# Kernel optimization log

Hardware: AMD Instinct MI355X
Metric: run time of the kernel (lower is better)

## Reference

```python
import jax, jax.numpy as jnp
import numpy as np

N_NODES = 100000


def _gcn_layer(h, W, b, src, dst, norm, n):
    # h: [N, Fin] -> transform then normalized scatter-add aggregation
    h = h @ W                                   # [N, Fout]
    msg = h[src] * norm[:, None]                # [E', Fout] gather + scale
    out = jax.ops.segment_sum(msg, dst, num_segments=n)  # scatter-add
    return out + b


def setup_inputs() -> dict:
    key = jax.random.key(0)
    k1, k2, k3, k4 = jax.random.split(key, 4)
    N, F_IN, HID, C, E = N_NODES, 512, 128, 40, 1600000
    x = jax.random.normal(k1, (N, F_IN), dtype=jnp.float32)
    edge_index = jax.random.randint(k2, (2, E), 0, N, dtype=jnp.int64)
    W1 = jax.random.normal(k3, (F_IN, HID), dtype=jnp.float32) * (1.0 / np.sqrt(F_IN))
    b1 = jnp.zeros((HID,), dtype=jnp.float32)
    W2 = jax.random.normal(k4, (HID, C), dtype=jnp.float32) * (1.0 / np.sqrt(HID))
    b2 = jnp.zeros((C,), dtype=jnp.float32)
    return {"x": x, "edge_index": edge_index, "W1": W1, "b1": b1, "W2": W2, "b2": b2}


def reference(x, edge_index, W1, b1, W2, b2):
    n = x.shape[0]
    # add self-loops (GCNConv default)
    loop = jnp.arange(n, dtype=edge_index.dtype)
    src = jnp.concatenate([edge_index[0], loop])
    dst = jnp.concatenate([edge_index[1], loop])
    # symmetric normalization: deg counted on destination (in-degree, incl. self-loop)
    deg = jax.ops.segment_sum(jnp.ones_like(dst, dtype=x.dtype), dst, num_segments=n)
    dis = jnp.where(deg > 0, jax.lax.rsqrt(deg), 0.0)  # deg^{-1/2}
    norm = dis[src] * dis[dst]                          # per-edge weight

    h = jax.nn.relu(_gcn_layer(x, W1, b1, src, dst, norm, n))
    # dropout: identity in eval mode (training=False)
    h = _gcn_layer(h, W2, b2, src, dst, norm, n)
    return jax.nn.log_softmax(h, axis=1)
```

## Files before the change

### kernel.cpp

```cpp
#include <hip/hip_runtime.h>
#include <hip/hip_bf16.h>


#define F_IN 512
#define HID  128
#define NC   40
#define NCP  48

typedef __attribute__((ext_vector_type(8))) short bf16x8;
typedef __attribute__((ext_vector_type(4))) float f32x4v;

__device__ __forceinline__ ushort f2bf(float f) {
    unsigned r;
    asm("v_cvt_pk_bf16_f32 %0, %1, %1" : "=v"(r) : "v"(f));
    return (ushort)r;
}
__device__ __forceinline__ unsigned cvtpk(float a, float b) {
    unsigned r;
    asm("v_cvt_pk_bf16_f32 %0, %1, %2" : "=v"(r) : "v"(a), "v"(b));
    return r;
}
__device__ __forceinline__ float bf2f(ushort u) {
    return __uint_as_float((unsigned)u << 16);
}
__device__ __forceinline__ bf16x8 cvt8(float4 lo, float4 hi) {
    union { unsigned u[4]; bf16x8 v; } t;
    t.u[0] = cvtpk(lo.x, lo.y); t.u[1] = cvtpk(lo.z, lo.w);
    t.u[2] = cvtpk(hi.x, hi.y); t.u[3] = cvtpk(hi.z, hi.w);
    return t.v;
}

__global__ void prep_k(const int* __restrict__ dst, int E, int EB,
                       unsigned* __restrict__ cnt, int* __restrict__ rank,
                       const float* __restrict__ W1, const float* __restrict__ W2,
                       ushort* __restrict__ W1p, ushort* __restrict__ W2p) {
    int b = blockIdx.x;
    if (b < EB) {
        int t = b * 256 + threadIdx.x;
        if (t < E) rank[t] = (int)atomicAdd(&cnt[dst[t]], 1u);
        return;
    }
    int t = (b - EB) * 256 + threadIdx.x;
    if (t < 65536) {
        int j = t & 7, n = (t >> 3) & 127, kb = (t >> 10) & 3, s = t >> 12;
        int k = s * 32 + kb * 8 + j;
        W1p[t] = f2bf(W1[(size_t)k * HID + n]);
    } else {
        int q = t - 65536;
        if (q < 6144) {
            int j = q & 7;
            int i2 = q >> 3;
            int n = i2 % 48;
            int i3 = i2 / 48;
            int kb = i3 & 3, ks = i3 >> 2;
            int k = ks * 32 + kb * 8 + j;
            float v = (n < NC) ? W2[(size_t)k * NC + n] : 0.f;
            W2p[q] = f2bf(v);
        }
    }
}

__global__ __launch_bounds__(1024) void scan_block(const unsigned* __restrict__ cnt,
                                                   unsigned* __restrict__ offs,
                                                   unsigned* __restrict__ bsums,
                                                   float* __restrict__ dis, int N) {
    int tid = threadIdx.x;
    int i = blockIdx.x * 1024 + tid;
    unsigned v = (i < N) ? cnt[i] : 0u;
    if (i < N) dis[i] = rsqrtf((float)v + 1.0f);
    int lane = tid & 63, w = tid >> 6;
    unsigned s = v;
    #pragma unroll
    for (int d = 1; d < 64; d <<= 1) {
        unsigned t = __shfl_up(s, d, 64);
        if (lane >= d) s += t;
    }
    __shared__ unsigned wt[16];
    if (lane == 63) wt[w] = s;
    __syncthreads();
    unsigned add = 0;
    #pragma unroll
    for (int j = 0; j < 16; j++) add += (j < w) ? wt[j] : 0u;
    unsigned incl = s + add;
    if (i < N) offs[i] = incl - v;
    if (tid == 1023) bsums[blockIdx.x] = incl;
}

__global__ __launch_bounds__(1024) void scan_add2(unsigned* __restrict__ offs,
                                                  const unsigned* __restrict__ bsums,
                                                  int N, unsigned total) {
    int i = blockIdx.x * 1024 + threadIdx.x;
    int lane = threadIdx.x & 63;
    unsigned s = 0;
    for (int j = lane; j < (int)blockIdx.x; j += 64) s += bsums[j];
    #pragma unroll
    for (int d = 1; d < 64; d <<= 1) s += __shfl_xor(s, d, 64);
    if (i < N) offs[i] += s;
    if (i == 0) offs[N] = total;
}

__global__ __launch_bounds__(256) void fill_gemm1(
        const int* __restrict__ src, const int* __restrict__ dst,
        const unsigned* __restrict__ offs, const int* __restrict__ rank,
        int* __restrict__ col, int E, int GB,
        const float* __restrict__ A, const ushort* __restrict__ Bp,
        const float* __restrict__ dis, ushort* __restrict__ C, int N) {
    if (blockIdx.x >= GB) {
        int t = (blockIdx.x - GB) * 256 + threadIdx.x;
        if (t < E) {
            int d = dst[t];
            col[offs[d] + (unsigned)rank[t]] = src[t];
        }
        return;
    }
    const int tid  = threadIdx.x;
    const int wave = tid >> 6;
    const int lane = tid & 63;
    const int quad = lane >> 4;
    const int mr   = lane & 15;
    const int base = (blockIdx.x * 4 + wave) * 16;
    if (base >= N) return;
    const int r0 = base + mr;
    const bool ok0 = r0 < N;
    const float* ap0 = A + (size_t)(ok0 ? r0 : 0) * F_IN + quad * 8;
    const ushort* bp = Bp + quad * 1024 + mr * 8;

    f32x4v acc0[8];
    #pragma unroll
    for (int t = 0; t < 8; t++) acc0[t] = (f32x4v){0.f, 0.f, 0.f, 0.f};

    float4 av[4][2];
    #pragma unroll
    for (int b = 0; b < 4; b++) {
        av[b][0] = *(const float4*)(ap0 + b * 32);
        av[b][1] = *(const float4*)(ap0 + b * 32 + 4);
    }

    #pragma unroll
    for (int s = 0; s < 16; s++) {
        bf16x8 fa0 = cvt8(av[s & 3][0], av[s & 3][1]);
        if (s < 12) {
            av[s & 3][0] = *(const float4*)(ap0 + (s + 4) * 32);
            av[s & 3][1] = *(const float4*)(ap0 + (s + 4) * 32 + 4);
        }
        const ushort* bs = bp + s * 4096;
        #pragma unroll
        for (int t = 0; t < 8; t++) {
            bf16x8 b = *(const bf16x8*)(bs + t * 128);
            acc0[t] = __builtin_amdgcn_mfma_f32_16x16x32_bf16(fa0, b, acc0[t], 0, 0, 0);
        }
    }

    #pragma unroll
    for (int rr = 0; rr < 4; rr++) {
        int ra = base + quad * 4 + rr;
        if (ra < N) {
            float ds = dis[ra];
            #pragma unroll
            for (int t = 0; t < 8; t++)
                C[(size_t)ra * HID + t * 16 + mr] = f2bf(acc0[t][rr] * ds);
        }
    }
}

__global__ __launch_bounds__(256) void agg1_k(const ushort* __restrict__ h,
                                              const int* __restrict__ col,
                                              const unsigned* __restrict__ offs,
                                              const float* __restrict__ dis,
                                              const float* __restrict__ b1,
                                              ushort* __restrict__ out, int N) {
    int node = blockIdx.x * 4 + (threadIdx.x >> 6);
    if (node >= N) return;
    int lane = threadIdx.x & 63;
    int ni = lane >> 4;
    int fl = lane & 15;
    const ushort* hb = h + (size_t)fl * 8;
    float a[8] = {0.f, 0.f, 0.f, 0.f, 0.f, 0.f, 0.f, 0.f};
    if (ni == 0) {
        uint4 v = *(const uint4*)(hb + (size_t)node * HID);
        const ushort* u = (const ushort*)&v;
        #pragma unroll
        for (int j = 0; j < 8; j++) a[j] = bf2f(u[j]);
    }
    unsigned p0 = offs[node], p1 = offs[node + 1];
    int sA = (p0 + ni     < p1) ? col[p0 + ni]     : -1;
    int sB = (p0 + ni + 4 < p1) ? col[p0 + ni + 4] : -1;
    for (unsigned p = p0; p < p1; p += 8) {
        int sC = (p + 8 + ni  < p1) ? col[p + 8 + ni]  : -1;
        int sD = (p + 12 + ni < p1) ? col[p + 12 + ni] : -1;
        if (sA >= 0) {
            uint4 v = *(const uint4*)(hb + (size_t)sA * HID);
            const ushort* u = (const ushort*)&v;
            #pragma unroll
            for (int j = 0; j < 8; j++) a[j] += bf2f(u[j]);
        }
        if (sB >= 0) {
            uint4 v = *(const uint4*)(hb + (size_t)sB * HID);
            const ushort* u = (const ushort*)&v;
            #pragma unroll
            for (int j = 0; j < 8; j++) a[j] += bf2f(u[j]);
        }
        sA = sC; sB = sD;
    }
    #pragma unroll
    for (int j = 0; j < 8; j++) {
        a[j] += __shfl_xor(a[j], 16);
        a[j] += __shfl_xor(a[j], 32);
    }
    if (ni == 0) {
        float dd = dis[node];
        float4 bb0 = *(const float4*)(b1 + fl * 8);
        float4 bb1 = *(const float4*)(b1 + fl * 8 + 4);
        const float bb[8] = {bb0.x, bb0.y, bb0.z, bb0.w, bb1.x, bb1.y, bb1.z, bb1.w};
        __align__(16) ushort o[8];
        #pragma unroll
        for (int j = 0; j < 8; j++) o[j] = f2bf(fmaxf(a[j] * dd + bb[j], 0.f));
        *(uint4*)(out + (size_t)node * HID + (size_t)fl * 8) = *(const uint4*)o;
    }
}

__global__ __launch_bounds__(256) void gemm2_mfma(const ushort* __restrict__ A,
                                                  const ushort* __restrict__ W2p,
                                                  const float* __restrict__ dis,
                                                  ushort* __restrict__ h2, int N) {
    const int tid  = threadIdx.x;
    const int wave = tid >> 6;
    const int lane = tid & 63;
    const int quad = lane >> 4;
    const int mr   = lane & 15;
    const int base = (blockIdx.x * 4 + wave) * 32;
    if (base >= N) return;
    const int r0 = base + mr;
    const int r1 = base + 16 + mr;
    const bool ok0 = r0 < N, ok1 = r1 < N;
    const ushort* ap0 = A + (size_t)(ok0 ? r0 : 0) * HID + quad * 8;
    const ushort* ap1 = A + (size_t)(ok1 ? r1 : 0) * HID + quad * 8;
    const ushort* bp = W2p + quad * 384 + mr * 8;

    f32x4v acc0[3], acc1[3];
    #pragma unroll
    for (int t = 0; t < 3; t++) {
        acc0[t] = (f32x4v){0.f, 0.f, 0.f, 0.f};
        acc1[t] = (f32x4v){0.f, 0.f, 0.f, 0.f};
    }
    #pragma unroll
    for (int ks = 0; ks < 4; ks++) {
        bf16x8 a0 = *(const bf16x8*)(ap0 + ks * 32);
        bf16x8 a1 = *(const bf16x8*)(ap1 + ks * 32);
        #pragma unroll
        for (int t = 0; t < 3; t++) {
            bf16x8 b = *(const bf16x8*)(bp + ks * 1536 + t * 128);
            acc0[t] = __builtin_amdgcn_mfma_f32_16x16x32_bf16(a0, b, acc0[t], 0, 0, 0);
            acc1[t] = __builtin_amdgcn_mfma_f32_16x16x32_bf16(a1, b, acc1[t], 0, 0, 0);
        }
    }
    #pragma unroll
    for (int rr = 0; rr < 4; rr++) {
        int ra = base + quad * 4 + rr;
        if (ra < N) {
            float ds = dis[ra];
            #pragma unroll
            for (int t = 0; t < 3; t++) {
                int c = t * 16 + mr;
                if (c < NC) h2[(size_t)ra * NCP + c] = f2bf(acc0[t][rr] * ds);
            }
        }
        int rb = base + 16 + quad * 4 + rr;
        if (rb < N) {
            float ds = dis[rb];
            #pragma unroll
            for (int t = 0; t < 3; t++) {
                int c = t * 16 + mr;
                if (c < NC) h2[(size_t)rb * NCP + c] = f2bf(acc1[t][rr] * ds);
            }
        }
    }
}

__global__ __launch_bounds__(256) void agg2_ls(const ushort* __restrict__ h2,
                                               const int* __restrict__ col,
                                               const unsigned* __restrict__ offs,
                                               const float* __restrict__ dis,
                                               const float* __restrict__ b2,
                                               float* __restrict__ out, int N) {
    int node = blockIdx.x * 4 + (threadIdx.x >> 6);
    if (node >= N) return;
    int lane = threadIdx.x & 63;
    int ni = lane >> 3;
    int fl = lane & 7;
    const bool act = fl < 5;
    const ushort* hb = h2 + (size_t)fl * 8;
    float a[8] = {0.f, 0.f, 0.f, 0.f, 0.f, 0.f, 0.f, 0.f};
    if (ni == 0 && act) {
        uint4 v = *(const uint4*)(hb + (size_t)node * NCP);
        const ushort* u = (const ushort*)&v;
        #pragma unroll
        for (int j = 0; j < 8; j++) a[j] = bf2f(u[j]);
    }
    unsigned p0 = offs[node], p1 = offs[node + 1];
    int sA = (p0 + ni     < p1) ? col[p0 + ni]     : -1;
    int sB = (p0 + ni + 8 < p1) ? col[p0 + ni + 8] : -1;
    for (unsigned p = p0; p < p1; p += 16) {
        int sC = (p + 16 + ni < p1) ? col[p + 16 + ni] : -1;
        int sD = (p + 24 + ni < p1) ? col[p + 24 + ni] : -1;
        if (sA >= 0 && act) {
            uint4 v = *(const uint4*)(hb + (size_t)sA * NCP);
            const ushort* u = (const ushort*)&v;
            #pragma unroll
            for (int j = 0; j < 8; j++) a[j] += bf2f(u[j]);
        }
        if (sB >= 0 && act) {
            uint4 v = *(const uint4*)(hb + (size_t)sB * NCP);
            const ushort* u = (const ushort*)&v;
            #pragma unroll
            for (int j = 0; j < 8; j++) a[j] += bf2f(u[j]);
        }
        sA = sC; sB = sD;
    }
    #pragma unroll
    for (int j = 0; j < 8; j++) {
        a[j] += __shfl_xor(a[j], 8);
        a[j] += __shfl_xor(a[j], 16);
        a[j] += __shfl_xor(a[j], 32);
    }
    float dd = dis[node];
    float l[8];
    float m = -1e30f;
    if (act) {
        #pragma unroll
        for (int j = 0; j < 8; j++) {
            l[j] = a[j] * dd + b2[fl * 8 + j];
            m = fmaxf(m, l[j]);
        }
    }
    #pragma unroll
    for (int d = 1; d < 8; d <<= 1) m = fmaxf(m, __shfl_xor(m, d, 8));
    float s = 0.f;
    if (act) {
        #pragma unroll
        for (int j = 0; j < 8; j++) s += __expf(l[j] - m);
    }
    #pragma unroll
    for (int d = 1; d < 8; d <<= 1) s += __shfl_xor(s, d, 8);
    float lse = m + __logf(s);
    if (ni == 0 && act) {
        float* op = out + (size_t)node * NC + fl * 8;
        *(float4*)op       = make_float4(l[0]-lse, l[1]-lse, l[2]-lse, l[3]-lse);
        *(float4*)(op + 4) = make_float4(l[4]-lse, l[5]-lse, l[6]-lse, l[7]-lse);
    }
}

extern "C" void kernel_launch(void* const* d_in, const int* in_sizes, int n_in,
                              void* d_out, int out_size, void* d_ws, size_t ws_size,
                              hipStream_t stream) {
    const float* x  = (const float*)d_in[0];
    const int*   ei = (const int*)d_in[1];
    const float* W1 = (const float*)d_in[2];
    const float* b1 = (const float*)d_in[3];
    const float* W2 = (const float*)d_in[4];
    const float* b2 = (const float*)d_in[5];
    float* out = (float*)d_out;

    const int N = in_sizes[0] / F_IN;
    const int E = in_sizes[1] / 2;
    const int* src = ei;
    const int* dst = ei + E;

    char* ws = (char*)d_ws;
    size_t o = 0;
    unsigned* cnt  = (unsigned*)(ws + o); o += (size_t)N * 4;
    float*    dis  = (float*)   (ws + o); o += (size_t)N * 4;
    unsigned* offs = (unsigned*)(ws + o); o += (size_t)(N + 4) * 4;
    unsigned* bsums= (unsigned*)(ws + o); o += 4096;
    int*      rank = (int*)     (ws + o); o += (size_t)E * 4;
    int*      col  = (int*)     (ws + o); o += (size_t)E * 4;
    o = (o + 15) & ~(size_t)15;
    ushort*   W1p  = (ushort*)  (ws + o); o += (size_t)F_IN * HID * 2;
    o = (o + 15) & ~(size_t)15;
    ushort*   W2p  = (ushort*)  (ws + o); o += 6144 * 2;
    o = (o + 15) & ~(size_t)15;
    ushort*   h1   = (ushort*)  (ws + o); o += (size_t)N * HID * 2;
    o = (o + 15) & ~(size_t)15;
    ushort*   ag1  = (ushort*)  (ws + o); o += (size_t)N * HID * 2;
    o = (o + 15) & ~(size_t)15;
    ushort*   h2   = (ushort*)  (ws + o); o += (size_t)N * NCP * 2;

    const int nb = (N + 1023) / 1024;
    const int EB = (E + 255) / 256;
    const int PB = (65536 + 6144 + 255) / 256;
    const int GB = (N + 63) / 64;

    hipMemsetAsync(cnt, 0, (size_t)N * 4, stream);
    prep_k<<<EB + PB, 256, 0, stream>>>(dst, E, EB, cnt, rank, W1, W2, W1p, W2p);
    scan_block<<<nb, 1024, 0, stream>>>(cnt, offs, bsums, dis, N);
    scan_add2<<<nb, 1024, 0, stream>>>(offs, bsums, N, (unsigned)E);

    fill_gemm1<<<GB + EB, 256, 0, stream>>>(src, dst, offs, rank, col, E, GB,
                                            x, W1p, dis, h1, N);

    agg1_k<<<(N + 3) / 4, 256, 0, stream>>>(h1, col, offs, dis, b1, ag1, N);

    gemm2_mfma<<<(N + 127) / 128, 256, 0, stream>>>(ag1, W2p, dis, h2, N);
    agg2_ls<<<(N + 3) / 4, 256, 0, stream>>>(h2, col, offs, dis, b2, out, N);
}
```

Measured before the change: 586.2 us.

## Interleave GEMM and CSR-fill blocks, batch A loads, branchless 4-way gather

```diff
diff --git a/kernel.cpp b/kernel.cpp
--- a/kernel.cpp
+++ b/kernel.cpp
@@ -99,14 +99,19 @@
     if (i == 0) offs[N] = total;
 }
 
-__global__ __launch_bounds__(256) void fill_gemm1(
+__global__ __launch_bounds__(256, 3) void fill_gemm1(
         const int* __restrict__ src, const int* __restrict__ dst,
         const unsigned* __restrict__ offs, const int* __restrict__ rank,
         int* __restrict__ col, int E, int GB,
         const float* __restrict__ A, const ushort* __restrict__ Bp,
         const float* __restrict__ dis, ushort* __restrict__ C, int N) {
-    if (blockIdx.x >= GB) {
-        int t = (blockIdx.x - GB) * 256 + threadIdx.x;
+    const int bid = blockIdx.x;
+    const int g   = bid / 5;
+    const int r5  = bid - g * 5;
+    if (!(r5 == 0 && g < GB)) {
+        int gb_before = g + (r5 > 0 ? 1 : 0);
+        if (gb_before > GB) gb_before = GB;
+        int t = (bid - gb_before) * 256 + threadIdx.x;
         if (t < E) {
             int d = dst[t];
             col[offs[d] + (unsigned)rank[t]] = src[t];
@@ -118,36 +123,35 @@
     const int lane = tid & 63;
     const int quad = lane >> 4;
     const int mr   = lane & 15;
-    const int base = (blockIdx.x * 4 + wave) * 16;
+    const int base = (g * 4 + wave) * 16;
     if (base >= N) return;
     const int r0 = base + mr;
-    const bool ok0 = r0 < N;
-    const float* ap0 = A + (size_t)(ok0 ? r0 : 0) * F_IN + quad * 8;
+    const float* ap0 = A + (size_t)(r0 < N ? r0 : 0) * F_IN + quad * 8;
     const ushort* bp = Bp + quad * 1024 + mr * 8;
 
     f32x4v acc0[8];
     #pragma unroll
     for (int t = 0; t < 8; t++) acc0[t] = (f32x4v){0.f, 0.f, 0.f, 0.f};
 
-    float4 av[4][2];
-    #pragma unroll
-    for (int b = 0; b < 4; b++) {
-        av[b][0] = *(const float4*)(ap0 + b * 32);
-        av[b][1] = *(const float4*)(ap0 + b * 32 + 4);
-    }
-
-    #pragma unroll
-    for (int s = 0; s < 16; s++) {
-        bf16x8 fa0 = cvt8(av[s & 3][0], av[s & 3][1]);
-        if (s < 12) {
-            av[s & 3][0] = *(const float4*)(ap0 + (s + 4) * 32);
-            av[s & 3][1] = *(const float4*)(ap0 + (s + 4) * 32 + 4);
-        }
-        const ushort* bs = bp + s * 4096;
-        #pragma unroll
-        for (int t = 0; t < 8; t++) {
-            bf16x8 b = *(const bf16x8*)(bs + t * 128);
-            acc0[t] = __builtin_amdgcn_mfma_f32_16x16x32_bf16(fa0, b, acc0[t], 0, 0, 0);
+    #pragma unroll 1
+    for (int h = 0; h < 2; h++) {
+        float4 av[8][2];
+        #pragma unroll
+        for (int q = 0; q < 8; q++) {
+            av[q][0] = *(const float4*)(ap0 + (h * 8 + q) * 32);
+            av[q][1] = *(const float4*)(ap0 + (h * 8 + q) * 32 + 4);
+        }
+        bf16x8 af[8];
+        #pragma unroll
+        for (int q = 0; q < 8; q++) af[q] = cvt8(av[q][0], av[q][1]);
+        #pragma unroll
+        for (int s2 = 0; s2 < 8; s2++) {
+            const ushort* bs = bp + (h * 8 + s2) * 4096;
+            #pragma unroll
+            for (int t = 0; t < 8; t++) {
+                bf16x8 bb = *(const bf16x8*)(bs + t * 128);
+                acc0[t] = __builtin_amdgcn_mfma_f32_16x16x32_bf16(af[s2], bb, acc0[t], 0, 0, 0);
+            }
         }
     }
 
@@ -183,24 +187,35 @@
         for (int j = 0; j < 8; j++) a[j] = bf2f(u[j]);
     }
     unsigned p0 = offs[node], p1 = offs[node + 1];
-    int sA = (p0 + ni     < p1) ? col[p0 + ni]     : -1;
-    int sB = (p0 + ni + 4 < p1) ? col[p0 + ni + 4] : -1;
-    for (unsigned p = p0; p < p1; p += 8) {
-        int sC = (p + 8 + ni  < p1) ? col[p + 8 + ni]  : -1;
-        int sD = (p + 12 + ni < p1) ? col[p + 12 + ni] : -1;
-        if (sA >= 0) {
-            uint4 v = *(const uint4*)(hb + (size_t)sA * HID);
-            const ushort* u = (const ushort*)&v;
-            #pragma unroll
-            for (int j = 0; j < 8; j++) a[j] += bf2f(u[j]);
-        }
-        if (sB >= 0) {
-            uint4 v = *(const uint4*)(hb + (size_t)sB * HID);
-            const ushort* u = (const ushort*)&v;
-            #pragma unroll
-            for (int j = 0; j < 8; j++) a[j] += bf2f(u[j]);
-        }
-        sA = sC; sB = sD;
+    int s0, s1, s2, s3;
+    float w0, w1, w2, w3;
+    #define GETC1(pos, sv, wv) { unsigned q_ = (pos); bool v_ = q_ < p1; \
+        sv = v_ ? col[q_] : 0; wv = v_ ? 1.f : 0.f; }
+    GETC1(p0 + ni,      s0, w0);
+    GETC1(p0 + ni + 4,  s1, w1);
+    GETC1(p0 + ni + 8,  s2, w2);
+    GETC1(p0 + ni + 12, s3, w3);
+    for (unsigned p = p0; p < p1; p += 16) {
+        int n0, n1, n2, n3;
+        float x0, x1, x2, x3;
+        GETC1(p + 16 + ni, n0, x0);
+        GETC1(p + 20 + ni, n1, x1);
+        GETC1(p + 24 + ni, n2, x2);
+        GETC1(p + 28 + ni, n3, x3);
+        uint4 v0 = *(const uint4*)(hb + (size_t)s0 * HID);
+        uint4 v1 = *(const uint4*)(hb + (size_t)s1 * HID);
+        uint4 v2 = *(const uint4*)(hb + (size_t)s2 * HID);
+        uint4 v3 = *(const uint4*)(hb + (size_t)s3 * HID);
+        const ushort* u0 = (const ushort*)&v0;
+        const ushort* u1 = (const ushort*)&v1;
+        const ushort* u2 = (const ushort*)&v2;
+        const ushort* u3 = (const ushort*)&v3;
+        #pragma unroll
+        for (int j = 0; j < 8; j++)
+            a[j] += (w0 * bf2f(u0[j]) + w1 * bf2f(u1[j]))
+                  + (w2 * bf2f(u2[j]) + w3 * bf2f(u3[j]));
+        s0 = n0; w0 = x0; s1 = n1; w1 = x1;
+        s2 = n2; w2 = x2; s3 = n3; w3 = x3;
     }
     #pragma unroll
     for (int j = 0; j < 8; j++) {
@@ -298,24 +313,35 @@
         for (int j = 0; j < 8; j++) a[j] = bf2f(u[j]);
     }
     unsigned p0 = offs[node], p1 = offs[node + 1];
-    int sA = (p0 + ni     < p1) ? col[p0 + ni]     : -1;
-    int sB = (p0 + ni + 8 < p1) ? col[p0 + ni + 8] : -1;
-    for (unsigned p = p0; p < p1; p += 16) {
-        int sC = (p + 16 + ni < p1) ? col[p + 16 + ni] : -1;
-        int sD = (p + 24 + ni < p1) ? col[p + 24 + ni] : -1;
-        if (sA >= 0 && act) {
-            uint4 v = *(const uint4*)(hb + (size_t)sA * NCP);
-            const ushort* u = (const ushort*)&v;
+    int s0, s1, s2, s3;
+    float w0, w1, w2, w3;
+    GETC1(p0 + ni,      s0, w0);
+    GETC1(p0 + ni + 8,  s1, w1);
+    GETC1(p0 + ni + 16, s2, w2);
+    GETC1(p0 + ni + 24, s3, w3);
+    for (unsigned p = p0; p < p1; p += 32) {
+        int n0, n1, n2, n3;
+        float x0, x1, x2, x3;
+        GETC1(p + 32 + ni, n0, x0);
+        GETC1(p + 40 + ni, n1, x1);
+        GETC1(p + 48 + ni, n2, x2);
+        GETC1(p + 56 + ni, n3, x3);
+        if (act) {
+            uint4 v0 = *(const uint4*)(hb + (size_t)s0 * NCP);
+            uint4 v1 = *(const uint4*)(hb + (size_t)s1 * NCP);
+            uint4 v2 = *(const uint4*)(hb + (size_t)s2 * NCP);
+            uint4 v3 = *(const uint4*)(hb + (size_t)s3 * NCP);
+            const ushort* u0 = (const ushort*)&v0;
+            const ushort* u1 = (const ushort*)&v1;
+            const ushort* u2 = (const ushort*)&v2;
+            const ushort* u3 = (const ushort*)&v3;
             #pragma unroll
-            for (int j = 0; j < 8; j++) a[j] += bf2f(u[j]);
-        }
-        if (sB >= 0 && act) {
-            uint4 v = *(const uint4*)(hb + (size_t)sB * NCP);
-            const ushort* u = (const ushort*)&v;
-            #pragma unroll
-            for (int j = 0; j < 8; j++) a[j] += bf2f(u[j]);
-        }
-        sA = sC; sB = sD;
+            for (int j = 0; j < 8; j++)
+                a[j] += (w0 * bf2f(u0[j]) + w1 * bf2f(u1[j]))
+                      + (w2 * bf2f(u2[j]) + w3 * bf2f(u3[j]));
+        }
+        s0 = n0; w0 = x0; s1 = n1; w1 = x1;
+        s2 = n2; w2 = x2; s3 = n3; w3 = x3;
     }
     #pragma unroll
     for (int j = 0; j < 8; j++) {
```

After: 587.4 us. Within noise of the previous version (+0.2%).
